# Kernel optimization log

Hardware: AMD Instinct MI355X
Metric: run time of the kernel (lower is better)

The kernel has to match this reference:

```python
import jax, jax.numpy as jnp
import numpy as np

N, E, DIN, DOUT = 40000, 640000, 128, 10


def _gat_layer(h_in, src, dst, W, a_src, a_dst, b, n_nodes):
    # h: [N, D]; edges include self-loops already
    h = h_in @ W
    alpha = jax.nn.leaky_relu((h @ a_src)[src] + (h @ a_dst)[dst], 0.2)  # [E']
    m = jax.ops.segment_max(alpha, dst, num_segments=n_nodes)
    e = jnp.exp(alpha - m[dst])
    s = jax.ops.segment_sum(e, dst, num_segments=n_nodes)
    coef = e / (s[dst] + 1e-16)
    out = jax.ops.segment_sum(h[src] * coef[:, None], dst, num_segments=n_nodes)
    return out + b


def setup_inputs() -> dict:
    key = jax.random.key(0)
    ks = jax.random.split(key, 20)
    p = lambda k, shp: (jax.random.normal(k, shp, dtype=jnp.float32) * 0.05)
    inp = {
        "x": jax.random.normal(ks[0], (N, DIN), dtype=jnp.float32),
        "edge_index": jax.random.randint(ks[1], (2, E), 0, N, dtype=jnp.int32),
        "batch": jnp.sort(jax.random.randint(ks[2], (N,), 0, 64, dtype=jnp.int32)),
        "edge_attr": jax.random.normal(ks[3], (E, 4), dtype=jnp.float32),
        # GATConv 1: 128 -> 64
        "W1": p(ks[4], (DIN, 64)), "a1s": p(ks[5], (64,)), "a1d": p(ks[6], (64,)), "b1": jnp.zeros((64,), jnp.float32),
        # GATConv 2: 64 -> 128
        "W2": p(ks[7], (64, 128)), "a2s": p(ks[8], (128,)), "a2d": p(ks[9], (128,)), "b2": jnp.zeros((128,), jnp.float32),
        # GATConv 3: 128 -> 128
        "W3": p(ks[10], (128, 128)), "a3s": p(ks[11], (128,)), "a3d": p(ks[12], (128,)), "b3": jnp.zeros((128,), jnp.float32),
        # SAGPooling scorer: GraphConv(128, 1)
        "wp_rel": p(ks[13], (128, 1)), "wp_root": p(ks[14], (128, 1)), "bp": jnp.zeros((1,), jnp.float32),
        # final Linear(128, out_channels)
        "Wl": p(ks[15], (128, DOUT)), "bl": jnp.zeros((DOUT,), jnp.float32),
    }
    return inp


def reference(x, edge_index, batch, edge_attr,
              W1, a1s, a1d, b1, W2, a2s, a2d, b2, W3, a3s, a3d, b3,
              wp_rel, wp_root, bp, Wl, bl):
    n = x.shape[0]
    src, dst = edge_index[0], edge_index[1]
    # GATConv adds self-loops (edge_attr unused: edge_dim=None)
    loops = jnp.arange(n, dtype=src.dtype)
    src_sl = jnp.concatenate([src, loops])
    dst_sl = jnp.concatenate([dst, loops])

    h = jax.nn.relu(_gat_layer(x, src_sl, dst_sl, W1, a1s, a1d, b1, n))
    h = jax.nn.relu(_gat_layer(h, src_sl, dst_sl, W2, a2s, a2d, b2, n))
    h = jax.nn.relu(_gat_layer(h, src_sl, dst_sl, W3, a3s, a3d, b3, n))

    # SAGPooling(ratio=1): score via GraphConv (no self-loops), tanh gating, all nodes kept
    agg = jax.ops.segment_sum(h[src], dst, num_segments=n)  # [N, 128]
    score = (agg @ wp_rel + h @ wp_root + bp)[:, 0]         # [N]
    h = h * jnp.tanh(score)[:, None]

    # dropout is identity in eval mode
    return jax.nn.relu(h @ Wl + bl)
```

## Files before the change

kernel.cpp:

```cpp
#include <hip/hip_runtime.h>
#include <math.h>

template<int K, int N>
__global__ __launch_bounds__(2 * N) void gemm_rt(
    const float* __restrict__ A, const float* __restrict__ B,
    float* __restrict__ C, int M,
    const float* __restrict__ iva, const float* __restrict__ ivb,
    float* __restrict__ ioa, float* __restrict__ iob,
    const float* __restrict__ ebias,
    const float* __restrict__ eva, const float* __restrict__ evb,
    float* __restrict__ eoa, float* __restrict__ eob)
{
    constexpr int KC = 32;
    constexpr int NC = K / KC;
    constexpr int TC = N / 8;
    constexpr int NT = 2 * N;
    constexpr int KT = KC / TC;
    constexpr int AST = 68;
    constexpr int A_F4 = 512 / NT;
    constexpr int B_F4 = 4;

    __shared__ float AsT[KC * AST];
    __shared__ float Bs[KC * N];

    const int tid = threadIdx.x;
    const int base = blockIdx.x * 64;
    const int tc = tid % TC;
    const int tr = tid / TC;

    float acc[4][8];
#pragma unroll
    for (int m = 0; m < 4; ++m)
#pragma unroll
        for (int j = 0; j < 8; ++j) acc[m][j] = 0.f;
    float sa[4], sb[4];
#pragma unroll
    for (int m = 0; m < 4; ++m) { sa[m] = 0.f; sb[m] = 0.f; }

    float4 ra[A_F4], rb[B_F4];

#pragma unroll
    for (int j = 0; j < A_F4; ++j) {
        int i = tid + j * NT; int row = i >> 3; int q = i & 7;
        int gr = base + row;
        ra[j] = (gr < M) ? *(const float4*)(A + (size_t)gr * K + 4 * q)
                         : make_float4(0.f, 0.f, 0.f, 0.f);
    }
#pragma unroll
    for (int j = 0; j < B_F4; ++j) {
        int i = tid + j * NT; int kk_ = i / (N / 4); int c4 = i % (N / 4);
        rb[j] = *(const float4*)(B + (size_t)kk_ * N + 4 * c4);
    }

    for (int ch = 0; ch < NC; ++ch) {
#pragma unroll
        for (int j = 0; j < A_F4; ++j) {
            int i = tid + j * NT; int row = i >> 3; int q = i & 7;
            AsT[(4 * q + 0) * AST + row] = ra[j].x;
            AsT[(4 * q + 1) * AST + row] = ra[j].y;
            AsT[(4 * q + 2) * AST + row] = ra[j].z;
            AsT[(4 * q + 3) * AST + row] = ra[j].w;
        }
#pragma unroll
        for (int j = 0; j < B_F4; ++j) {
            int i = tid + j * NT; int kk_ = i / (N / 4); int c4 = i % (N / 4);
            *(float4*)(Bs + kk_ * N + 4 * c4) = rb[j];
        }
        __syncthreads();

        if (ch + 1 < NC) {
            const int k0 = (ch + 1) * KC;
#pragma unroll
            for (int j = 0; j < A_F4; ++j) {
                int i = tid + j * NT; int row = i >> 3; int q = i & 7;
                int gr = base + row;
                ra[j] = (gr < M) ? *(const float4*)(A + (size_t)gr * K + k0 + 4 * q)
                                 : make_float4(0.f, 0.f, 0.f, 0.f);
            }
#pragma unroll
            for (int j = 0; j < B_F4; ++j) {
                int i = tid + j * NT; int kk_ = i / (N / 4); int c4 = i % (N / 4);
                rb[j] = *(const float4*)(B + (size_t)(k0 + kk_) * N + 4 * c4);
            }
        }

#pragma unroll 8
        for (int kk = 0; kk < KC; ++kk) {
            float4 a0 = *(const float4*)(AsT + kk * AST + 4 * tr);
            const float* bp = Bs + kk * N + 8 * tc;
            float4 b0 = *(const float4*)(bp);
            float4 b1 = *(const float4*)(bp + 4);
#pragma unroll
            for (int m = 0; m < 4; ++m) {
                float av = ((const float*)&a0)[m];
                acc[m][0] = fmaf(av, b0.x, acc[m][0]);
                acc[m][1] = fmaf(av, b0.y, acc[m][1]);
                acc[m][2] = fmaf(av, b0.z, acc[m][2]);
                acc[m][3] = fmaf(av, b0.w, acc[m][3]);
                acc[m][4] = fmaf(av, b1.x, acc[m][4]);
                acc[m][5] = fmaf(av, b1.y, acc[m][5]);
                acc[m][6] = fmaf(av, b1.z, acc[m][6]);
                acc[m][7] = fmaf(av, b1.w, acc[m][7]);
            }
        }

        if (iva != nullptr) {
            const int k0 = ch * KC;
#pragma unroll
            for (int kl = 0; kl < KT; ++kl) {
                int k = tc * KT + kl;
                float av_ = iva[k0 + k];
                float bv_ = ivb[k0 + k];
#pragma unroll
                for (int m = 0; m < 4; ++m) {
                    float aval = AsT[k * AST + 4 * tr + m];
                    sa[m] = fmaf(aval, av_, sa[m]);
                    sb[m] = fmaf(aval, bv_, sb[m]);
                }
            }
        }
        __syncthreads();
    }

    float pa[4], pb[4];
#pragma unroll
    for (int m = 0; m < 4; ++m) { pa[m] = 0.f; pb[m] = 0.f; }
#pragma unroll
    for (int m = 0; m < 4; ++m) {
        int gr = base + 4 * tr + m;
        float o[8];
#pragma unroll
        for (int j = 0; j < 8; ++j) o[j] = acc[m][j];
        if (ebias != nullptr) {
#pragma unroll
            for (int j = 0; j < 8; ++j) o[j] = fmaxf(o[j] + ebias[8 * tc + j], 0.f);
        }
        if (gr < M) {
            *(float4*)(C + (size_t)gr * N + 8 * tc) = make_float4(o[0], o[1], o[2], o[3]);
            *(float4*)(C + (size_t)gr * N + 8 * tc + 4) = make_float4(o[4], o[5], o[6], o[7]);
        }
        if (eva != nullptr) {
#pragma unroll
            for (int j = 0; j < 8; ++j) {
                pa[m] = fmaf(o[j], eva[8 * tc + j], pa[m]);
                pb[m] = fmaf(o[j], evb[8 * tc + j], pb[m]);
            }
        }
    }
    if (eva != nullptr) {
#pragma unroll
        for (int m = 0; m < 4; ++m) {
#pragma unroll
            for (int off = TC / 2; off; off >>= 1) {
                pa[m] += __shfl_xor(pa[m], off);
                pb[m] += __shfl_xor(pb[m], off);
            }
        }
        if (tc == 0) {
#pragma unroll
            for (int m = 0; m < 4; ++m) {
                int gr = base + 4 * tr + m;
                if (gr < M) { eoa[gr] = pa[m]; eob[gr] = pb[m]; }
            }
        }
    }
    if (iva != nullptr) {
#pragma unroll
        for (int m = 0; m < 4; ++m) {
#pragma unroll
            for (int off = TC / 2; off; off >>= 1) {
                sa[m] += __shfl_xor(sa[m], off);
                sb[m] += __shfl_xor(sb[m], off);
            }
        }
        if (tc == 0) {
#pragma unroll
            for (int m = 0; m < 4; ++m) {
                int gr = base + 4 * tr + m;
                if (gr < M) { ioa[gr] = sa[m]; iob[gr] = sb[m]; }
            }
        }
    }
}

template<int K, int N, int NT>
__global__ __launch_bounds__(256) void gemm_tile(
    const float* __restrict__ A, const float* __restrict__ B,
    float* __restrict__ C, int M,
    const float* __restrict__ bias, const float* __restrict__ score, int outN)
{
    __shared__ float As[64 * K];
    const int tid = threadIdx.x;
    const int base = blockIdx.x * 64;
    for (int idx = tid; idx < 64 * K; idx += 256) {
        int r = idx / K, k = idx - r * K;
        int gr = base + r;
        As[idx] = (gr < M) ? A[(size_t)gr * K + k] : 0.f;
    }
    __syncthreads();
    constexpr int RSTEP = 256 / NT;
    constexpr int NR = 64 / RSTEP;
    const int c = tid % NT;
    const int r0 = tid / NT;
    float acc[NR];
#pragma unroll
    for (int i = 0; i < NR; ++i) acc[i] = 0.f;
    const float4* As4 = reinterpret_cast<const float4*>(As);
    const float* Bc = B + c;
    float b0 = Bc[0 * N], b1 = Bc[1 * N], b2 = Bc[2 * N], b3 = Bc[3 * N];
    for (int k = 0; k < K; k += 4) {
        const int kn = (k + 4 < K) ? (k + 4) : k;
        float n0 = Bc[(kn + 0) * N];
        float n1 = Bc[(kn + 1) * N];
        float n2 = Bc[(kn + 2) * N];
        float n3 = Bc[(kn + 3) * N];
#pragma unroll
        for (int i = 0; i < NR; ++i) {
            float4 a = As4[((r0 + i * RSTEP) * K + k) >> 2];
            acc[i] = fmaf(a.x, b0, acc[i]);
            acc[i] = fmaf(a.y, b1, acc[i]);
            acc[i] = fmaf(a.z, b2, acc[i]);
            acc[i] = fmaf(a.w, b3, acc[i]);
        }
        b0 = n0; b1 = n1; b2 = n2; b3 = n3;
    }
    if (c < outN) {
#pragma unroll
        for (int i = 0; i < NR; ++i) {
            int gr = base + r0 + i * RSTEP;
            if (gr < M) {
                float v = tanhf(score[gr]) * acc[i] + bias[c];
                C[(size_t)gr * outN + c] = fmaxf(v, 0.f);
            }
        }
    }
}

__global__ __launch_bounds__(256) void hist_deg(
    const int* __restrict__ dst, int* __restrict__ deg, int E, int n)
{
    int e = blockIdx.x * 256 + threadIdx.x;
    if (e >= E + n) return;
    int d = (e < E) ? dst[e] : (e - E);
    atomicAdd(deg + d, 1);
}

__global__ __launch_bounds__(256) void scan_local(
    const int* __restrict__ deg, int* __restrict__ row_start, int* __restrict__ blocksum, int n)
{
    __shared__ int s[256];
    const int t = threadIdx.x;
    const int i = blockIdx.x * 256 + t;
    int v = (i < n) ? deg[i] : 0;
    s[t] = v;
    __syncthreads();
#pragma unroll
    for (int off = 1; off < 256; off <<= 1) {
        int u = (t >= off) ? s[t - off] : 0;
        __syncthreads();
        s[t] += u;
        __syncthreads();
    }
    if (i < n) row_start[i] = s[t] - v;
    if (t == 255) blocksum[blockIdx.x] = s[255];
}

__global__ __launch_bounds__(256) void scan_blocks(int* __restrict__ blocksum, int nb)
{
    __shared__ int s[256];
    const int t = threadIdx.x;
    int v = (t < nb) ? blocksum[t] : 0;
    s[t] = v;
    __syncthreads();
#pragma unroll
    for (int off = 1; off < 256; off <<= 1) {
        int u = (t >= off) ? s[t - off] : 0;
        __syncthreads();
        s[t] += u;
        __syncthreads();
    }
    if (t < nb) blocksum[t] = s[t] - v;
}

__global__ __launch_bounds__(256) void scan_add(
    int* __restrict__ row_start, int* __restrict__ cursor,
    const int* __restrict__ blocksum, int n, int total)
{
    const int i = blockIdx.x * 256 + threadIdx.x;
    if (i < n) {
        int v = row_start[i] + blocksum[blockIdx.x];
        row_start[i] = v;
        cursor[i] = v;
    } else if (i == n) {
        row_start[n] = total;
    }
}

__global__ __launch_bounds__(256) void fill_csr(
    const int* __restrict__ src, const int* __restrict__ dst,
    int* __restrict__ cursor, int* __restrict__ csr_src, int E, int n)
{
    int e = blockIdx.x * 256 + threadIdx.x;
    if (e >= E + n) return;
    int s, d;
    if (e < E) { s = src[e]; d = dst[e]; } else { s = d = e - E; }
    int pos = atomicAdd(cursor + d, 1);
    csr_src[pos] = s;
}

template<int D, bool POOL>
__global__ __launch_bounds__(256) void gat_aggregate(
    const int* __restrict__ row_start, const int* __restrict__ csr_src,
    const float* __restrict__ asv, const float* __restrict__ adv,
    const float* __restrict__ h, const float* __restrict__ bias,
    float* __restrict__ out,
    const float* __restrict__ wpr, const float* __restrict__ wpo,
    float* __restrict__ poolA, float* __restrict__ poolB, int n)
{
    __shared__ float lds_e[4][128];
    __shared__ int   lds_i[4][128];
    const int node = (blockIdx.x * 256 + threadIdx.x) >> 6;
    const int lane = threadIdx.x & 63;
    const int w = threadIdx.x >> 6;
    if (node >= n) return;
    const int beg = row_start[node];
    const int deg = row_start[node + 1] - beg;
    const float advv = adv[node];
    const bool fast = (deg <= 128);

    float amax = -INFINITY;
    if (fast) {
        for (int j = lane; j < deg; j += 64) {
            int s = csr_src[beg + j];
            lds_i[w][j] = s;
            float a = asv[s] + advv;
            a = (a >= 0.f) ? a : 0.2f * a;
            lds_e[w][j] = a;
            amax = fmaxf(amax, a);
        }
    } else {
        for (int j = lane; j < deg; j += 64) {
            float a = asv[csr_src[beg + j]] + advv;
            a = (a >= 0.f) ? a : 0.2f * a;
            amax = fmaxf(amax, a);
        }
    }
#pragma unroll
    for (int off = 32; off; off >>= 1) amax = fmaxf(amax, __shfl_xor(amax, off));

    float ssum = 0.f;
    if (fast) {
        for (int j = lane; j < deg; j += 64) {
            float ev = expf(lds_e[w][j] - amax);
            lds_e[w][j] = ev;
            ssum += ev;
        }
    } else {
        for (int j = lane; j < deg; j += 64) {
            float a = asv[csr_src[beg + j]] + advv;
            a = (a >= 0.f) ? a : 0.2f * a;
            ssum += expf(a - amax);
        }
    }
#pragma unroll
    for (int off = 32; off; off >>= 1) ssum += __shfl_xor(ssum, off);
    const float inv = 1.f / (ssum + 1e-16f);

    if (fast) {
        if constexpr (D == 128) {
            const float4* h4 = reinterpret_cast<const float4*>(h);
            const int half = lane >> 5;
            const int fl = lane & 31;
            float4 a0 = {0,0,0,0}, a1 = {0,0,0,0}, a2 = {0,0,0,0}, a3 = {0,0,0,0};
            int j = 0;
            for (; j + 8 <= deg; j += 8) {
                int e0 = j + half, e1 = j + 2 + half, e2 = j + 4 + half, e3 = j + 6 + half;
                int s0 = lds_i[w][e0], s1 = lds_i[w][e1], s2 = lds_i[w][e2], s3 = lds_i[w][e3];
                float c0 = lds_e[w][e0] * inv, c1 = lds_e[w][e1] * inv;
                float c2 = lds_e[w][e2] * inv, c3 = lds_e[w][e3] * inv;
                float4 v0 = h4[(size_t)s0 * 32 + fl];
                float4 v1 = h4[(size_t)s1 * 32 + fl];
                float4 v2 = h4[(size_t)s2 * 32 + fl];
                float4 v3 = h4[(size_t)s3 * 32 + fl];
                a0.x = fmaf(v0.x, c0, a0.x); a0.y = fmaf(v0.y, c0, a0.y);
                a0.z = fmaf(v0.z, c0, a0.z); a0.w = fmaf(v0.w, c0, a0.w);
                a1.x = fmaf(v1.x, c1, a1.x); a1.y = fmaf(v1.y, c1, a1.y);
                a1.z = fmaf(v1.z, c1, a1.z); a1.w = fmaf(v1.w, c1, a1.w);
                a2.x = fmaf(v2.x, c2, a2.x); a2.y = fmaf(v2.y, c2, a2.y);
                a2.z = fmaf(v2.z, c2, a2.z); a2.w = fmaf(v2.w, c2, a2.w);
                a3.x = fmaf(v3.x, c3, a3.x); a3.y = fmaf(v3.y, c3, a3.y);
                a3.z = fmaf(v3.z, c3, a3.z); a3.w = fmaf(v3.w, c3, a3.w);
            }
            for (; j < deg; j += 2) {
                int e = j + half;
                bool ok = (e < deg);
                int s = lds_i[w][ok ? e : 0];
                float c = ok ? lds_e[w][e] * inv : 0.f;
                float4 v = h4[(size_t)s * 32 + fl];
                a0.x = fmaf(v.x, c, a0.x); a0.y = fmaf(v.y, c, a0.y);
                a0.z = fmaf(v.z, c, a0.z); a0.w = fmaf(v.w, c, a0.w);
            }
            float4 t;
            t.x = (a0.x + a1.x) + (a2.x + a3.x);
            t.y = (a0.y + a1.y) + (a2.y + a3.y);
            t.z = (a0.z + a1.z) + (a2.z + a3.z);
            t.w = (a0.w + a1.w) + (a2.w + a3.w);
            t.x += __shfl_xor(t.x, 32);
            t.y += __shfl_xor(t.y, 32);
            t.z += __shfl_xor(t.z, 32);
            t.w += __shfl_xor(t.w, 32);
            const float4 b4 = reinterpret_cast<const float4*>(bias)[fl];
            float4 o;
            o.x = fmaxf(t.x + b4.x, 0.f);
            o.y = fmaxf(t.y + b4.y, 0.f);
            o.z = fmaxf(t.z + b4.z, 0.f);
            o.w = fmaxf(t.w + b4.w, 0.f);
            if (half == 0)
                reinterpret_cast<float4*>(out)[(size_t)node * 32 + fl] = o;
            if constexpr (POOL) {
                const float4 r4 = reinterpret_cast<const float4*>(wpr)[fl];
                const float4 q4 = reinterpret_cast<const float4*>(wpo)[fl];
                float pa = o.x * r4.x + o.y * r4.y + o.z * r4.z + o.w * r4.w;
                float pb = o.x * q4.x + o.y * q4.y + o.z * q4.z + o.w * q4.w;
#pragma unroll
                for (int off = 16; off; off >>= 1) {
                    pa += __shfl_xor(pa, off);
                    pb += __shfl_xor(pb, off);
                }
                if (lane == 0) { poolA[node] = pa; poolB[node] = pb; }
            }
        } else {
            const float4* h4 = reinterpret_cast<const float4*>(h);
            const int q = lane >> 4;
            const int fl = lane & 15;
            float4 a0 = {0,0,0,0}, a1 = {0,0,0,0};
            int j = 0;
            for (; j + 8 <= deg; j += 8) {
                int e0 = j + q, e1 = j + 4 + q;
                int s0 = lds_i[w][e0], s1 = lds_i[w][e1];
                float c0 = lds_e[w][e0] * inv, c1 = lds_e[w][e1] * inv;
                float4 v0 = h4[(size_t)s0 * 16 + fl];
                float4 v1 = h4[(size_t)s1 * 16 + fl];
                a0.x = fmaf(v0.x, c0, a0.x); a0.y = fmaf(v0.y, c0, a0.y);
                a0.z = fmaf(v0.z, c0, a0.z); a0.w = fmaf(v0.w, c0, a0.w);
                a1.x = fmaf(v1.x, c1, a1.x); a1.y = fmaf(v1.y, c1, a1.y);
                a1.z = fmaf(v1.z, c1, a1.z); a1.w = fmaf(v1.w, c1, a1.w);
            }
            for (; j < deg; j += 4) {
                int e = j + q;
                bool ok = (e < deg);
                int s = lds_i[w][ok ? e : 0];
                float c = ok ? lds_e[w][e] * inv : 0.f;
                float4 v = h4[(size_t)s * 16 + fl];
                a0.x = fmaf(v.x, c, a0.x); a0.y = fmaf(v.y, c, a0.y);
                a0.z = fmaf(v.z, c, a0.z); a0.w = fmaf(v.w, c, a0.w);
            }
            float4 t;
            t.x = a0.x + a1.x; t.y = a0.y + a1.y; t.z = a0.z + a1.z; t.w = a0.w + a1.w;
            t.x += __shfl_xor(t.x, 16); t.x += __shfl_xor(t.x, 32);
            t.y += __shfl_xor(t.y, 16); t.y += __shfl_xor(t.y, 32);
            t.z += __shfl_xor(t.z, 16); t.z += __shfl_xor(t.z, 32);
            t.w += __shfl_xor(t.w, 16); t.w += __shfl_xor(t.w, 32);
            const float4 b4 = reinterpret_cast<const float4*>(bias)[fl];
            float4 o;
            o.x = fmaxf(t.x + b4.x, 0.f);
            o.y = fmaxf(t.y + b4.y, 0.f);
            o.z = fmaxf(t.z + b4.z, 0.f);
            o.w = fmaxf(t.w + b4.w, 0.f);
            if (q == 0)
                reinterpret_cast<float4*>(out)[(size_t)node * 16 + fl] = o;
        }
    } else {
        if constexpr (D == 128) {
            const float2* h2 = reinterpret_cast<const float2*>(h);
            float2 a0 = {0.f, 0.f};
            for (int j = 0; j < deg; ++j) {
                int s = csr_src[beg + j];
                float a = asv[s] + advv;
                a = (a >= 0.f) ? a : 0.2f * a;
                float c = expf(a - amax) * inv;
                float2 v = h2[(size_t)s * 64 + lane];
                a0.x = fmaf(v.x, c, a0.x); a0.y = fmaf(v.y, c, a0.y);
            }
            float2 o;
            o.x = fmaxf(a0.x + bias[2 * lane], 0.f);
            o.y = fmaxf(a0.y + bias[2 * lane + 1], 0.f);
            reinterpret_cast<float2*>(out)[(size_t)node * 64 + lane] = o;
            if constexpr (POOL) {
                float pa = fmaf(o.x, wpr[2 * lane], o.y * wpr[2 * lane + 1]);
                float pb = fmaf(o.x, wpo[2 * lane], o.y * wpo[2 * lane + 1]);
#pragma unroll
                for (int off = 32; off; off >>= 1) {
                    pa += __shfl_xor(pa, off);
                    pb += __shfl_xor(pb, off);
                }
                if (lane == 0) { poolA[node] = pa; poolB[node] = pb; }
            }
        } else {
            float a0 = 0.f;
            for (int j = 0; j < deg; ++j) {
                int s = csr_src[beg + j];
                float a = asv[s] + advv;
                a = (a >= 0.f) ? a : 0.2f * a;
                float c = expf(a - amax) * inv;
                a0 = fmaf(h[(size_t)s * D + lane], c, a0);
            }
            out[(size_t)node * D + lane] = fmaxf(a0 + bias[lane], 0.f);
        }
    }
}

__global__ __launch_bounds__(256) void score_csr(
    const int* __restrict__ row_start, const int* __restrict__ csr_src,
    const float* __restrict__ ts, const float* __restrict__ td,
    const float* __restrict__ bp, float* __restrict__ score, int n)
{
    int i = blockIdx.x * 256 + threadIdx.x;
    if (i >= n) return;
    int beg = row_start[i], end = row_start[i + 1];
    float s = td[i] + bp[0] - ts[i];
    for (int j = beg; j < end; ++j) s += ts[csr_src[j]];
    score[i] = s;
}

__global__ __launch_bounds__(256) void precompute(
    const float* __restrict__ W1, const float* __restrict__ a1s, const float* __restrict__ a1d,
    const float* __restrict__ W2, const float* __restrict__ a2s, const float* __restrict__ a2d,
    const float* __restrict__ W3, const float* __restrict__ a3s, const float* __restrict__ a3d,
    const float* __restrict__ Wl, const float* __restrict__ bl,
    float* __restrict__ va1, float* __restrict__ vb1,
    float* __restrict__ va2, float* __restrict__ vb2,
    float* __restrict__ va3, float* __restrict__ vb3,
    float* __restrict__ Wlp, float* __restrict__ blp,
    int* __restrict__ deg, int n)
{
    int t = blockIdx.x * 256 + threadIdx.x;
    if (t < n) deg[t] = 0;
    if (t < 128) {
        float sa = 0.f, sb = 0.f;
        for (int j = 0; j < 64; ++j) {
            float w = W1[t * 64 + j];
            sa = fmaf(w, a1s[j], sa); sb = fmaf(w, a1d[j], sb);
        }
        va1[t] = sa; vb1[t] = sb;
    } else if (t < 192) {
        int k = t - 128;
        float sa = 0.f, sb = 0.f;
        for (int j = 0; j < 128; ++j) {
            float w = W2[k * 128 + j];
            sa = fmaf(w, a2s[j], sa); sb = fmaf(w, a2d[j], sb);
        }
        va2[k] = sa; vb2[k] = sb;
    } else if (t < 320) {
        int k = t - 192;
        float sa = 0.f, sb = 0.f;
        for (int j = 0; j < 128; ++j) {
            float w = W3[k * 128 + j];
            sa = fmaf(w, a3s[j], sa); sb = fmaf(w, a3d[j], sb);
        }
        va3[k] = sa; vb3[k] = sb;
    } else if (t < 320 + 2048) {
        int i = t - 320;
        int k = i >> 4, c = i & 15;
        Wlp[i] = (c < 10) ? Wl[k * 10 + c] : 0.f;
    } else if (t < 320 + 2048 + 16) {
        int c = t - (320 + 2048);
        blp[c] = (c < 10) ? bl[c] : 0.f;
    }
}

extern "C" void kernel_launch(void* const* d_in, const int* in_sizes, int n_in,
                              void* d_out, int out_size, void* d_ws, size_t ws_size,
                              hipStream_t stream) {
    const float* x   = (const float*)d_in[0];
    const int*   ei  = (const int*)d_in[1];
    const float* W1  = (const float*)d_in[4];
    const float* a1s = (const float*)d_in[5];
    const float* a1d = (const float*)d_in[6];
    const float* b1  = (const float*)d_in[7];
    const float* W2  = (const float*)d_in[8];
    const float* a2s = (const float*)d_in[9];
    const float* a2d = (const float*)d_in[10];
    const float* b2  = (const float*)d_in[11];
    const float* W3  = (const float*)d_in[12];
    const float* a3s = (const float*)d_in[13];
    const float* a3d = (const float*)d_in[14];
    const float* b3  = (const float*)d_in[15];
    const float* wpr = (const float*)d_in[16];
    const float* wpo = (const float*)d_in[17];
    const float* bp  = (const float*)d_in[18];
    const float* Wl  = (const float*)d_in[19];
    const float* bl  = (const float*)d_in[20];

    const int n = in_sizes[0] / 128;
    const int E = in_sizes[1] / 2;
    const int Esl = E + n;
    const int* src = ei;
    const int* dst = ei + E;

    float* ws = (float*)d_ws;
    const size_t nd = (size_t)n * 128;
    float* bufA      = ws;
    float* bufB      = bufA + nd;
    float* asv       = bufB + nd;
    float* adv       = asv + n;
    float* tsv       = adv + n;
    float* tdv       = tsv + n;
    float* score     = tdv + n;
    int*   deg       = (int*)(score + n);
    int*   row_start = deg + n;
    int*   cursor    = row_start + n + 1;
    int*   blocksum  = cursor + n;
    int*   csr_src   = blocksum + 256;
    float* va1       = (float*)(csr_src + Esl);
    float* vb1       = va1 + 128;
    float* va2       = vb1 + 128;
    float* vb2       = va2 + 64;
    float* va3       = vb2 + 64;
    float* vb3       = va3 + 128;
    float* Wlp       = vb3 + 128;
    float* blp       = Wlp + 128 * 16;

    const unsigned EB = (unsigned)((Esl + 255) / 256);
    const unsigned NB = (unsigned)((n + 255) / 256);
    const unsigned MB = (unsigned)((n + 63) / 64);
    const unsigned WB = (unsigned)(((size_t)n * 64 + 255) / 256);

    precompute<<<NB, 256, 0, stream>>>(W1, a1s, a1d, W2, a2s, a2d, W3, a3s, a3d, Wl, bl,
                                       va1, vb1, va2, vb2, va3, vb3, Wlp, blp, deg, n);
    hist_deg<<<EB, 256, 0, stream>>>(dst, deg, E, n);
    scan_local<<<NB, 256, 0, stream>>>(deg, row_start, blocksum, n);
    scan_blocks<<<1, 256, 0, stream>>>(blocksum, (int)NB);
    scan_add<<<NB, 256, 0, stream>>>(row_start, cursor, blocksum, n, Esl);
    fill_csr<<<EB, 256, 0, stream>>>(src, dst, cursor, csr_src, E, n);

    gemm_rt<128, 64><<<MB, 128, 0, stream>>>(
        x, W1, bufA, n, va1, vb1, asv, adv, nullptr, nullptr, nullptr, nullptr, nullptr);
    gat_aggregate<64, false><<<WB, 256, 0, stream>>>(row_start, csr_src, asv, adv, bufA, b1, bufB,
                                                     nullptr, nullptr, nullptr, nullptr, n);

    gemm_rt<64, 128><<<MB, 256, 0, stream>>>(
        bufB, W2, bufA, n, va2, vb2, asv, adv, nullptr, nullptr, nullptr, nullptr, nullptr);
    gat_aggregate<128, false><<<WB, 256, 0, stream>>>(row_start, csr_src, asv, adv, bufA, b2, bufB,
                                                      nullptr, nullptr, nullptr, nullptr, n);

    gemm_rt<128, 128><<<MB, 256, 0, stream>>>(
        bufB, W3, bufA, n, va3, vb3, asv, adv, nullptr, nullptr, nullptr, nullptr, nullptr);
    gat_aggregate<128, true><<<WB, 256, 0, stream>>>(row_start, csr_src, asv, adv, bufA, b3, bufB,
                                                     wpr, wpo, tsv, tdv, n);

    score_csr<<<NB, 256, 0, stream>>>(row_start, csr_src, tsv, tdv, bp, score, n);
    gemm_tile<128, 16, 16><<<MB, 256, 0, stream>>>(bufB, Wlp, (float*)d_out, n, blp, score, 10);
}
```

Before: 308.5 us.

## Handle self-loops implicitly, single-pass softmax, and split GEMM columns across blocks

Self-loop edges are no longer stored in the CSR. Each node's self term is computed directly in the aggregation kernel, and the score kernel drops its correction for it. The separate max-reduction pass in the attention softmax is removed, so exp is applied to the raw scores in one pass; this saves work but risks overflow if the scores become large. The 128-column GEMMs are split over blockIdx.y into 64-column tiles with 128-thread blocks to add parallelism. The attention-vector dot products are computed only in the y=0 blocks.

Measured after the change: 296.3 us, median of 3. -4.0%, faster.

```diff
diff --git a/kernel.cpp b/kernel.cpp
--- a/kernel.cpp
+++ b/kernel.cpp
@@ -1,30 +1,28 @@
 #include <hip/hip_runtime.h>
 #include <math.h>
 
-template<int K, int N>
-__global__ __launch_bounds__(2 * N) void gemm_rt(
+template<int K, int N, int CPB>
+__global__ __launch_bounds__(2 * CPB) void gemm_rt(
     const float* __restrict__ A, const float* __restrict__ B,
     float* __restrict__ C, int M,
     const float* __restrict__ iva, const float* __restrict__ ivb,
-    float* __restrict__ ioa, float* __restrict__ iob,
-    const float* __restrict__ ebias,
-    const float* __restrict__ eva, const float* __restrict__ evb,
-    float* __restrict__ eoa, float* __restrict__ eob)
+    float* __restrict__ ioa, float* __restrict__ iob)
 {
     constexpr int KC = 32;
     constexpr int NC = K / KC;
-    constexpr int TC = N / 8;
-    constexpr int NT = 2 * N;
+    constexpr int TC = CPB / 8;
+    constexpr int NT = 2 * CPB;
     constexpr int KT = KC / TC;
     constexpr int AST = 68;
     constexpr int A_F4 = 512 / NT;
-    constexpr int B_F4 = 4;
+    constexpr int B_F4 = (KC * CPB / 4) / NT;
 
     __shared__ float AsT[KC * AST];
-    __shared__ float Bs[KC * N];
+    __shared__ float Bs[KC * CPB];
 
     const int tid = threadIdx.x;
     const int base = blockIdx.x * 64;
+    const int col0 = blockIdx.y * CPB;
     const int tc = tid % TC;
     const int tr = tid / TC;
 
@@ -48,8 +46,8 @@
     }
 #pragma unroll
     for (int j = 0; j < B_F4; ++j) {
-        int i = tid + j * NT; int kk_ = i / (N / 4); int c4 = i % (N / 4);
-        rb[j] = *(const float4*)(B + (size_t)kk_ * N + 4 * c4);
+        int i = tid + j * NT; int kk_ = i / (CPB / 4); int c4 = i % (CPB / 4);
+        rb[j] = *(const float4*)(B + (size_t)kk_ * N + col0 + 4 * c4);
     }
 
     for (int ch = 0; ch < NC; ++ch) {
@@ -63,8 +61,8 @@
         }
 #pragma unroll
         for (int j = 0; j < B_F4; ++j) {
-            int i = tid + j * NT; int kk_ = i / (N / 4); int c4 = i % (N / 4);
-            *(float4*)(Bs + kk_ * N + 4 * c4) = rb[j];
+            int i = tid + j * NT; int kk_ = i / (CPB / 4); int c4 = i % (CPB / 4);
+            *(float4*)(Bs + kk_ * CPB + 4 * c4) = rb[j];
         }
         __syncthreads();
 
@@ -79,15 +77,15 @@
             }
 #pragma unroll
             for (int j = 0; j < B_F4; ++j) {
-                int i = tid + j * NT; int kk_ = i / (N / 4); int c4 = i % (N / 4);
-                rb[j] = *(const float4*)(B + (size_t)(k0 + kk_) * N + 4 * c4);
+                int i = tid + j * NT; int kk_ = i / (CPB / 4); int c4 = i % (CPB / 4);
+                rb[j] = *(const float4*)(B + (size_t)(k0 + kk_) * N + col0 + 4 * c4);
             }
         }
 
 #pragma unroll 8
         for (int kk = 0; kk < KC; ++kk) {
             float4 a0 = *(const float4*)(AsT + kk * AST + 4 * tr);
-            const float* bp = Bs + kk * N + 8 * tc;
+            const float* bp = Bs + kk * CPB + 8 * tc;
             float4 b0 = *(const float4*)(bp);
             float4 b1 = *(const float4*)(bp + 4);
 #pragma unroll
@@ -104,7 +102,7 @@
             }
         }
 
-        if (iva != nullptr) {
+        if (iva != nullptr && blockIdx.y == 0) {
             const int k0 = ch * KC;
 #pragma unroll
             for (int kl = 0; kl < KT; ++kl) {
@@ -122,49 +120,17 @@
         __syncthreads();
     }
 
-    float pa[4], pb[4];
-#pragma unroll
-    for (int m = 0; m < 4; ++m) { pa[m] = 0.f; pb[m] = 0.f; }
 #pragma unroll
     for (int m = 0; m < 4; ++m) {
         int gr = base + 4 * tr + m;
-        float o[8];
-#pragma unroll
-        for (int j = 0; j < 8; ++j) o[j] = acc[m][j];
-        if (ebias != nullptr) {
-#pragma unroll
-            for (int j = 0; j < 8; ++j) o[j] = fmaxf(o[j] + ebias[8 * tc + j], 0.f);
-        }
         if (gr < M) {
-            *(float4*)(C + (size_t)gr * N + 8 * tc) = make_float4(o[0], o[1], o[2], o[3]);
-            *(float4*)(C + (size_t)gr * N + 8 * tc + 4) = make_float4(o[4], o[5], o[6], o[7]);
-        }
-        if (eva != nullptr) {
-#pragma unroll
-            for (int j = 0; j < 8; ++j) {
-                pa[m] = fmaf(o[j], eva[8 * tc + j], pa[m]);
-                pb[m] = fmaf(o[j], evb[8 * tc + j], pb[m]);
-            }
-        }
-    }
-    if (eva != nullptr) {
-#pragma unroll
-        for (int m = 0; m < 4; ++m) {
-#pragma unroll
-            for (int off = TC / 2; off; off >>= 1) {
-                pa[m] += __shfl_xor(pa[m], off);
-                pb[m] += __shfl_xor(pb[m], off);
-            }
-        }
-        if (tc == 0) {
-#pragma unroll
-            for (int m = 0; m < 4; ++m) {
-                int gr = base + 4 * tr + m;
-                if (gr < M) { eoa[gr] = pa[m]; eob[gr] = pb[m]; }
-            }
-        }
-    }
-    if (iva != nullptr) {
+            *(float4*)(C + (size_t)gr * N + col0 + 8 * tc) =
+                make_float4(acc[m][0], acc[m][1], acc[m][2], acc[m][3]);
+            *(float4*)(C + (size_t)gr * N + col0 + 8 * tc + 4) =
+                make_float4(acc[m][4], acc[m][5], acc[m][6], acc[m][7]);
+        }
+    }
+    if (iva != nullptr && blockIdx.y == 0) {
 #pragma unroll
         for (int m = 0; m < 4; ++m) {
 #pragma unroll
@@ -237,12 +203,10 @@
 }
 
 __global__ __launch_bounds__(256) void hist_deg(
-    const int* __restrict__ dst, int* __restrict__ deg, int E, int n)
+    const int* __restrict__ dst, int* __restrict__ deg, int E)
 {
     int e = blockIdx.x * 256 + threadIdx.x;
-    if (e >= E + n) return;
-    int d = (e < E) ? dst[e] : (e - E);
-    atomicAdd(deg + d, 1);
+    if (e < E) atomicAdd(deg + dst[e], 1);
 }
 
 __global__ __launch_bounds__(256) void scan_local(
@@ -298,14 +262,12 @@
 
 __global__ __launch_bounds__(256) void fill_csr(
     const int* __restrict__ src, const int* __restrict__ dst,
-    int* __restrict__ cursor, int* __restrict__ csr_src, int E, int n)
+    int* __restrict__ cursor, int* __restrict__ csr_src, int E)
 {
     int e = blockIdx.x * 256 + threadIdx.x;
-    if (e >= E + n) return;
-    int s, d;
-    if (e < E) { s = src[e]; d = dst[e]; } else { s = d = e - E; }
-    int pos = atomicAdd(cursor + d, 1);
-    csr_src[pos] = s;
+    if (e >= E) return;
+    int pos = atomicAdd(cursor + dst[e], 1);
+    csr_src[pos] = src[e];
 }
 
 template<int D, bool POOL>
@@ -328,38 +290,26 @@
     const float advv = adv[node];
     const bool fast = (deg <= 128);
 
-    float amax = -INFINITY;
+    float a_self = asv[node] + advv;
+    a_self = (a_self >= 0.f) ? a_self : 0.2f * a_self;
+    const float ev_self = expf(a_self);
+
+    float ssum = (lane == 0) ? ev_self : 0.f;
     if (fast) {
         for (int j = lane; j < deg; j += 64) {
             int s = csr_src[beg + j];
             lds_i[w][j] = s;
             float a = asv[s] + advv;
             a = (a >= 0.f) ? a : 0.2f * a;
-            lds_e[w][j] = a;
-            amax = fmaxf(amax, a);
+            float ev = expf(a);
+            lds_e[w][j] = ev;
+            ssum += ev;
         }
     } else {
         for (int j = lane; j < deg; j += 64) {
             float a = asv[csr_src[beg + j]] + advv;
             a = (a >= 0.f) ? a : 0.2f * a;
-            amax = fmaxf(amax, a);
-        }
-    }
-#pragma unroll
-    for (int off = 32; off; off >>= 1) amax = fmaxf(amax, __shfl_xor(amax, off));
-
-    float ssum = 0.f;
-    if (fast) {
-        for (int j = lane; j < deg; j += 64) {
-            float ev = expf(lds_e[w][j] - amax);
-            lds_e[w][j] = ev;
-            ssum += ev;
-        }
-    } else {
-        for (int j = lane; j < deg; j += 64) {
-            float a = asv[csr_src[beg + j]] + advv;
-            a = (a >= 0.f) ? a : 0.2f * a;
-            ssum += expf(a - amax);
+            ssum += expf(a);
         }
     }
 #pragma unroll
@@ -400,6 +350,12 @@
                 a0.x = fmaf(v.x, c, a0.x); a0.y = fmaf(v.y, c, a0.y);
                 a0.z = fmaf(v.z, c, a0.z); a0.w = fmaf(v.w, c, a0.w);
             }
+            {
+                float c = (half == 0) ? ev_self * inv : 0.f;
+                float4 v = h4[(size_t)node * 32 + fl];
+                a1.x = fmaf(v.x, c, a1.x); a1.y = fmaf(v.y, c, a1.y);
+                a1.z = fmaf(v.z, c, a1.z); a1.w = fmaf(v.w, c, a1.w);
+            }
             float4 t;
             t.x = (a0.x + a1.x) + (a2.x + a3.x);
             t.y = (a0.y + a1.y) + (a2.y + a3.y);
@@ -455,6 +411,12 @@
                 a0.x = fmaf(v.x, c, a0.x); a0.y = fmaf(v.y, c, a0.y);
                 a0.z = fmaf(v.z, c, a0.z); a0.w = fmaf(v.w, c, a0.w);
             }
+            {
+                float c = (q == 0) ? ev_self * inv : 0.f;
+                float4 v = h4[(size_t)node * 16 + fl];
+                a1.x = fmaf(v.x, c, a1.x); a1.y = fmaf(v.y, c, a1.y);
+                a1.z = fmaf(v.z, c, a1.z); a1.w = fmaf(v.w, c, a1.w);
+            }
             float4 t;
             t.x = a0.x + a1.x; t.y = a0.y + a1.y; t.z = a0.z + a1.z; t.w = a0.w + a1.w;
             t.x += __shfl_xor(t.x, 16); t.x += __shfl_xor(t.x, 32);
@@ -478,8 +440,13 @@
                 int s = csr_src[beg + j];
                 float a = asv[s] + advv;
                 a = (a >= 0.f) ? a : 0.2f * a;
-                float c = expf(a - amax) * inv;
+                float c = expf(a) * inv;
                 float2 v = h2[(size_t)s * 64 + lane];
+                a0.x = fmaf(v.x, c, a0.x); a0.y = fmaf(v.y, c, a0.y);
+            }
+            {
+                float c = ev_self * inv;
+                float2 v = h2[(size_t)node * 64 + lane];
                 a0.x = fmaf(v.x, c, a0.x); a0.y = fmaf(v.y, c, a0.y);
             }
             float2 o;
@@ -502,9 +469,9 @@
                 int s = csr_src[beg + j];
                 float a = asv[s] + advv;
                 a = (a >= 0.f) ? a : 0.2f * a;
-                float c = expf(a - amax) * inv;
-                a0 = fmaf(h[(size_t)s * D + lane], c, a0);
-            }
+                a0 = fmaf(h[(size_t)s * D + lane], expf(a) * inv, a0);
+            }
+            a0 = fmaf(h[(size_t)node * D + lane], ev_self * inv, a0);
             out[(size_t)node * D + lane] = fmaxf(a0 + bias[lane], 0.f);
         }
     }
@@ -518,7 +485,7 @@
     int i = blockIdx.x * 256 + threadIdx.x;
     if (i >= n) return;
     int beg = row_start[i], end = row_start[i + 1];
-    float s = td[i] + bp[0] - ts[i];
+    float s = td[i] + bp[0];
     for (int j = beg; j < end; ++j) s += ts[csr_src[j]];
     score[i] = s;
 }
@@ -594,7 +561,6 @@
 
     const int n = in_sizes[0] / 128;
     const int E = in_sizes[1] / 2;
-    const int Esl = E + n;
     const int* src = ei;
     const int* dst = ei + E;
 
@@ -612,7 +578,7 @@
     int*   cursor    = row_start + n + 1;
     int*   blocksum  = cursor + n;
     int*   csr_src   = blocksum + 256;
-    float* va1       = (float*)(csr_src + Esl);
+    float* va1       = (float*)(csr_src + E);
     float* vb1       = va1 + 128;
     float* va2       = vb1 + 128;
     float* vb2       = va2 + 64;
@@ -621,31 +587,31 @@
     float* Wlp       = vb3 + 128;
     float* blp       = Wlp + 128 * 16;
 
-    const unsigned EB = (unsigned)((Esl + 255) / 256);
+    const unsigned EB = (unsigned)((E + 255) / 256);
     const unsigned NB = (unsigned)((n + 255) / 256);
     const unsigned MB = (unsigned)((n + 63) / 64);
     const unsigned WB = (unsigned)(((size_t)n * 64 + 255) / 256);
 
     precompute<<<NB, 256, 0, stream>>>(W1, a1s, a1d, W2, a2s, a2d, W3, a3s, a3d, Wl, bl,
                                        va1, vb1, va2, vb2, va3, vb3, Wlp, blp, deg, n);
-    hist_deg<<<EB, 256, 0, stream>>>(dst, deg, E, n);
+    hist_deg<<<EB, 256, 0, stream>>>(dst, deg, E);
     scan_local<<<NB, 256, 0, stream>>>(deg, row_start, blocksum, n);
     scan_blocks<<<1, 256, 0, stream>>>(blocksum, (int)NB);
-    scan_add<<<NB, 256, 0, stream>>>(row_start, cursor, blocksum, n, Esl);
-    fill_csr<<<EB, 256, 0, stream>>>(src, dst, cursor, csr_src, E, n);
-
-    gemm_rt<128, 64><<<MB, 128, 0, stream>>>(
-        x, W1, bufA, n, va1, vb1, asv, adv, nullptr, nullptr, nullptr, nullptr, nullptr);
+    scan_add<<<NB, 256, 0, stream>>>(row_start, cursor, blocksum, n, E);
+    fill_csr<<<EB, 256, 0, stream>>>(src, dst, cursor, csr_src, E);
+
+    gemm_rt<128, 64, 64><<<dim3(MB, 1), 128, 0, stream>>>(
+        x, W1, bufA, n, va1, vb1, asv, adv);
     gat_aggregate<64, false><<<WB, 256, 0, stream>>>(row_start, csr_src, asv, adv, bufA, b1, bufB,
                                                      nullptr, nullptr, nullptr, nullptr, n);
 
-    gemm_rt<64, 128><<<MB, 256, 0, stream>>>(
-        bufB, W2, bufA, n, va2, vb2, asv, adv, nullptr, nullptr, nullptr, nullptr, nullptr);
+    gemm_rt<64, 128, 64><<<dim3(MB, 2), 128, 0, stream>>>(
+        bufB, W2, bufA, n, va2, vb2, asv, adv);
     gat_aggregate<128, false><<<WB, 256, 0, stream>>>(row_start, csr_src, asv, adv, bufA, b2, bufB,
                                                       nullptr, nullptr, nullptr, nullptr, n);
 
-    gemm_rt<128, 128><<<MB, 256, 0, stream>>>(
-        bufB, W3, bufA, n, va3, vb3, asv, adv, nullptr, nullptr, nullptr, nullptr, nullptr);
+    gemm_rt<128, 128, 64><<<dim3(MB, 2), 128, 0, stream>>>(
+        bufB, W3, bufA, n, va3, vb3, asv, adv);
     gat_aggregate<128, true><<<WB, 256, 0, stream>>>(row_start, csr_src, asv, adv, bufA, b3, bufB,
                                                      wpr, wpo, tsv, tdv, n);
 
```
